# Kernel optimization log

Hardware: AMD Instinct MI355X
Metric: run time of the kernel (lower is better)

## Reference

```python
import jax, jax.numpy as jnp
import numpy as np

N = 50000       # nodes
E = 800000      # edges (before self-loops)
IN_DIM = 256
HIDDEN = 256
HEADS = 4
C1 = HIDDEN // HEADS  # 64 per-head channels in layer 1
OUT_DIM = 128
NEG_SLOPE = 0.2  # PyG GATConv default negative_slope


def setup_inputs() -> dict:
    key = jax.random.key(0)
    ks = jax.random.split(key, 10)
    x = jax.random.normal(ks[0], (N, IN_DIM), dtype=jnp.float32) * 0.1
    edge_index = jax.random.randint(ks[1], (2, E), 0, N, dtype=jnp.int64)
    # layer 1 params (GATConv: lin weight, att_src, att_dst, bias)
    W1 = jax.random.normal(ks[2], (IN_DIM, HEADS * C1), dtype=jnp.float32) * 0.05
    att_src1 = jax.random.normal(ks[3], (HEADS, C1), dtype=jnp.float32) * 0.05
    att_dst1 = jax.random.normal(ks[4], (HEADS, C1), dtype=jnp.float32) * 0.05
    bias1 = jnp.zeros((HEADS * C1,), dtype=jnp.float32)
    # layer 2 params (heads=1, concat=False)
    W2 = jax.random.normal(ks[5], (HIDDEN, OUT_DIM), dtype=jnp.float32) * 0.05
    att_src2 = jax.random.normal(ks[6], (1, OUT_DIM), dtype=jnp.float32) * 0.05
    att_dst2 = jax.random.normal(ks[7], (1, OUT_DIM), dtype=jnp.float32) * 0.05
    bias2 = jnp.zeros((OUT_DIM,), dtype=jnp.float32)
    return {"x": x, "edge_index": edge_index, "W1": W1, "att_src1": att_src1,
            "att_dst1": att_dst1, "bias1": bias1, "W2": W2, "att_src2": att_src2,
            "att_dst2": att_dst2, "bias2": bias2}


def gat_conv(x, src, dst, W, a_src, a_dst, bias, concat):
    # x: [N, F_in]; src/dst: [E'] (self-loops included); W: [F_in, H*C]
    H, C = a_src.shape
    h = (x @ W).reshape(-1, H, C)                      # [N, H, C]
    alpha_s = (h * a_src[None]).sum(-1)                # [N, H]
    alpha_d = (h * a_dst[None]).sum(-1)                # [N, H]
    e = jax.nn.leaky_relu(alpha_s[src] + alpha_d[dst], NEG_SLOPE)  # [E', H]
    # segment softmax over incoming edges of each destination node
    emax = jax.ops.segment_max(e, dst, num_segments=N)             # [N, H]
    ex = jnp.exp(e - emax[dst])
    denom = jax.ops.segment_sum(ex, dst, num_segments=N)           # [N, H]
    alpha = ex / (denom[dst] + 1e-16)                              # [E', H]
    msg = h[src] * alpha[:, :, None]                               # [E', H, C]
    out = jax.ops.segment_sum(msg, dst, num_segments=N)            # [N, H, C]
    if concat:
        out = out.reshape(N, H * C)
    else:
        out = out.mean(axis=1)
    return out + bias


def reference(x, edge_index, W1, att_src1, att_dst1, bias1, W2, att_src2, att_dst2, bias2):
    # PyG GATConv add_self_loops=True
    loops = jnp.arange(N, dtype=edge_index.dtype)
    src = jnp.concatenate([edge_index[0], loops])
    dst = jnp.concatenate([edge_index[1], loops])
    h = gat_conv(x, src, dst, W1, att_src1, att_dst1, bias1, concat=True)   # [N, 256]
    h = jax.nn.gelu(h, approximate=False)  # torch F.gelu default = exact erf
    # dropout inactive in eval mode
    out = gat_conv(h, src, dst, W2, att_src2, att_dst2, bias2, concat=False)  # [N, 128]
    return out
```

## Files before the change

### kernel.cpp

```cpp
#include <hip/hip_runtime.h>
#include <hip/hip_bf16.h>


#define IN_DIM   256
#define HID      256
#define HEADS    4
#define C1       64
#define OUT_DIM  128
#define NEG_SLOPE 0.2f

using short8 = __attribute__((ext_vector_type(8))) short;
using f32x4  = __attribute__((ext_vector_type(4))) float;
using uint2n = __attribute__((ext_vector_type(2))) unsigned int;

__device__ __forceinline__ float loadf(const void* p, size_t i, int isbf16) {
    return isbf16 ? __bfloat162float(((const __hip_bfloat16*)p)[i])
                  : ((const float*)p)[i];
}

__device__ __forceinline__ float leaky(float a) {
    return a > 0.f ? a : NEG_SLOPE * a;
}

__device__ __forceinline__ unsigned short f2bs(float f) {
    __hip_bfloat16 b = __float2bfloat16(f);
    return *reinterpret_cast<unsigned short*>(&b);
}

__device__ __forceinline__ float blo(unsigned u) {
    return __uint_as_float(u << 16);
}
__device__ __forceinline__ float bhi(unsigned u) {
    return __uint_as_float(u & 0xffff0000u);
}

__device__ __forceinline__ float gelu(float c) {
    return 0.5f * c * (1.0f + erff(c * 0.70710678f));
}


__global__ void prep_kernel(const void* x, int nx,
                            const void* W1, const void* as1w, const void* ad1w,
                            const void* b1, const void* W2, const void* as2w,
                            const void* ad2w, const void* b2,
                            float* as1wf, float* ad1wf, float* b1f,
                            float* as2wf, float* ad2wf, float* b2f,
                            int* flags) {
    const void* srcs[9] = {x, W1, as1w, ad1w, b1, W2, as2w, ad2w, b2};
    int ns[9] = {nx, IN_DIM * HID, HEADS * C1, HEADS * C1, HID,
                 HID * OUT_DIM, OUT_DIM, OUT_DIM, OUT_DIM};
    float* dsts[9] = {nullptr, nullptr, as1wf, ad1wf, b1f, nullptr, as2wf, ad2wf, b2f};

    int b = blockIdx.x;
    const unsigned short* u = (const unsigned short*)srcs[b];
    int n = ns[b];
    int nslots = n < 4096 ? n : 4096;
    int cnt = 0;
    for (int i = threadIdx.x; i < nslots; i += 256) {
        unsigned short a = u[i] & 0x7FFF;
        int e = a >> 7;
        if (a == 0 || (e >= 90 && e <= 140)) cnt++;
    }
    __shared__ int red[4];
    __shared__ int flagS;
    for (int o = 32; o > 0; o >>= 1) cnt += __shfl_down(cnt, o);
    if ((threadIdx.x & 63) == 0) red[threadIdx.x >> 6] = cnt;
    __syncthreads();
    if (threadIdx.x == 0) {
        int tot = red[0] + red[1] + red[2] + red[3];
        int f = (tot * 10 >= nslots * 8) ? 1 : 0;
        flags[b] = f;
        flagS = f;
    }
    __syncthreads();
    int f = flagS;
    float* d = dsts[b];
    if (d) {
        for (int i = threadIdx.x; i < n; i += 256) d[i] = loadf(srcs[b], i, f);
    }
}

__global__ void tpose_kernel(const void* W1, const void* W2,
                             const int* flags,
                             __hip_bfloat16* __restrict__ W1T,
                             __hip_bfloat16* __restrict__ W2T,
                             int* __restrict__ deg, int n) {
    int b = blockIdx.x;
    int t = threadIdx.x;
    int gi = b * 256 + t;
    if (gi < n) deg[gi] = 0;
    if (b < 256) {
        int i = b * 256 + t;
        int k = i >> 8, nn = i & 255;
        W1T[nn * 256 + k] = __float2bfloat16(loadf(W1, i, flags[1]));
    } else {
        int i = (b - 256) * 256 + t;
        int k = i >> 7, nn = i & 127;
        W2T[nn * 256 + k] = __float2bfloat16(loadf(W2, i, flags[5]));
    }
}


__global__ void count_kernel(const int* __restrict__ ei, int E, int EP,
                             int* __restrict__ deg) {
    int idx = blockIdx.x * blockDim.x + threadIdx.x;
    if (idx >= EP) return;
    int d = (idx < E) ? ei[E + idx] : (idx - E);
    atomicAdd(&deg[d], 1);
}

__global__ __launch_bounds__(256) void psum_kernel(const int* __restrict__ deg,
                                                   int* __restrict__ bsum, int n) {
    int i = blockIdx.x * 256 + threadIdx.x;
    int v = (i < n) ? deg[i] : 0;
#pragma unroll
    for (int o = 32; o > 0; o >>= 1) v += __shfl_down(v, o);
    __shared__ int red[4];
    if ((threadIdx.x & 63) == 0) red[threadIdx.x >> 6] = v;
    __syncthreads();
    if (threadIdx.x == 0) bsum[blockIdx.x] = red[0] + red[1] + red[2] + red[3];
}

__global__ __launch_bounds__(256) void wscan_kernel(int* __restrict__ deg,
                                                    const int* __restrict__ bsum,
                                                    int* __restrict__ offs,
                                                    float* __restrict__ z0,
                                                    float* __restrict__ z1,
                                                    int n) {
    __shared__ int sh[256];
    __shared__ int red[4];
    int b = blockIdx.x;
    int t = threadIdx.x;

    int pref = 0;
    for (int i = t; i < b; i += 256) pref += bsum[i];
#pragma unroll
    for (int o = 32; o > 0; o >>= 1) pref += __shfl_down(pref, o);
    if ((t & 63) == 0) red[t >> 6] = pref;
    __syncthreads();
    int bpref = red[0] + red[1] + red[2] + red[3];

    int i = b * 256 + t;
    int v = (i < n) ? deg[i] : 0;
    sh[t] = v;
    __syncthreads();
    for (int d = 1; d < 256; d <<= 1) {
        int u = (t >= d) ? sh[t - d] : 0;
        __syncthreads();
        sh[t] += u;
        __syncthreads();
    }
    int excl = sh[t] - v + bpref;
    if (i < n) {
        offs[i] = excl;
        deg[i]  = excl;
        z0[i] = 0.f;
        z1[i] = 0.f;
        if (i == n - 1) offs[n] = excl + v;
    }
}

__global__ void fill_kernel(const int* __restrict__ ei, int E, int EP,
                            int* __restrict__ cursor, int* __restrict__ ssrc,
                            int* __restrict__ sdst) {
    int idx = blockIdx.x * blockDim.x + threadIdx.x;
    if (idx >= EP) return;
    int src = (idx < E) ? ei[idx]     : (idx - E);
    int dst = (idx < E) ? ei[E + idx] : (idx - E);
    int pos = atomicAdd(&cursor[dst], 1);
    ssrc[pos] = src;
    sdst[pos] = dst;
}


__device__ __forceinline__ void store_out(float* C, size_t i, float v) { C[i] = v; }
__device__ __forceinline__ void store_out(__hip_bfloat16* C, size_t i, float v) {
    C[i] = __float2bfloat16(v);
}

template <typename OutT>
__global__ __launch_bounds__(256) void gemm_mfma(
    const void* __restrict__ A0, const int* aflagp,
    const __hip_bfloat16* __restrict__ BT,
    OutT* __restrict__ C, int M, int Nn, int K,
    const float* __restrict__ aswp, const float* __restrict__ adwp,
    float* __restrict__ asO, float* __restrict__ adO, int hstride) {
    constexpr int BM = 128, BN = 128, BK = 32;
    constexpr int LDK = BK + 8;
    __shared__ __hip_bfloat16 As[BM * LDK];
    __shared__ __hip_bfloat16 Bs[BN * LDK];

    const int Mb = (M + BM - 1) / BM;
    const int Nb = Nn / BN;
    int bmi, bni;
    if (Nb == 2) {
        int L = blockIdx.x;
        bmi = (L >> 4) * 8 + (L & 7);
        bni = (L >> 3) & 1;
        if (bmi >= Mb) return;
    } else {
        bmi = blockIdx.x;
        bni = 0;
        if (bmi >= Mb) return;
    }

    const int aflag = aflagp ? *aflagp : 1;
    const int tid  = threadIdx.x;
    const int lane = tid & 63;
    const int wv   = tid >> 6;
    const int wm   = (wv >> 1) * 64;
    const int wn   = (wv & 1) * 64;
    const int l15  = lane & 15;
    const int quad = lane >> 4;

    const int bm = bmi * BM;
    const int bn = bni * BN;

    f32x4 acc[4][4] = {};

    for (int k0 = 0; k0 < K; k0 += BK) {
#pragma unroll
        for (int i = 0; i < 2; ++i) {
            int c    = tid + i * 256;
            int row  = c >> 2;
            int koff = (c & 3) * 8;
            int grow = bm + row;
            short8 av = {};
            if (grow < M) {
                if (aflag) {
                    av = *(const short8*)((const __hip_bfloat16*)A0 +
                                          (size_t)grow * K + k0 + koff);
                } else {
                    const float* ap = (const float*)A0 + (size_t)grow * K + k0 + koff;
                    float4 f0 = *(const float4*)ap;
                    float4 f1 = *(const float4*)(ap + 4);
                    av[0] = (short)f2bs(f0.x); av[1] = (short)f2bs(f0.y);
                    av[2] = (short)f2bs(f0.z); av[3] = (short)f2bs(f0.w);
                    av[4] = (short)f2bs(f1.x); av[5] = (short)f2bs(f1.y);
                    av[6] = (short)f2bs(f1.z); av[7] = (short)f2bs(f1.w);
                }
            }
            *(short8*)&As[row * LDK + koff] = av;
            short8 bv = *(const short8*)(BT + (size_t)(bn + row) * K + k0 + koff);
            *(short8*)&Bs[row * LDK + koff] = bv;
        }
        __syncthreads();

        short8 af[4], bf[4];
#pragma unroll
        for (int f = 0; f < 4; ++f) {
            af[f] = *(const short8*)&As[(wm + f * 16 + l15) * LDK + quad * 8];
            bf[f] = *(const short8*)&Bs[(wn + f * 16 + l15) * LDK + quad * 8];
        }
#pragma unroll
        for (int fm = 0; fm < 4; ++fm)
#pragma unroll
            for (int fn = 0; fn < 4; ++fn)
                acc[fm][fn] = __builtin_amdgcn_mfma_f32_16x16x32_bf16(
                    af[fm], bf[fn], acc[fm][fn], 0, 0, 0);
        __syncthreads();
    }

#pragma unroll
    for (int fm = 0; fm < 4; ++fm) {
#pragma unroll
        for (int r = 0; r < 4; ++r) {
            int grow = bm + wm + fm * 16 + quad * 4 + r;
            if (grow >= M) continue;
#pragma unroll
            for (int fn = 0; fn < 4; ++fn) {
                int gcol = bn + wn + fn * 16 + l15;
                store_out(C, (size_t)grow * Nn + gcol, acc[fm][fn][r]);
            }
        }
    }

    if (aswp) {
        float aw[4], dw[4];
#pragma unroll
        for (int fn = 0; fn < 4; ++fn) {
            int gcol = bn + wn + fn * 16 + l15;
            aw[fn] = aswp[gcol];
            dw[fn] = adwp[gcol];
        }
        int head = (bn + wn) >> 6;
#pragma unroll
        for (int fm = 0; fm < 4; ++fm) {
#pragma unroll
            for (int r = 0; r < 4; ++r) {
                int grow = bm + wm + fm * 16 + quad * 4 + r;
                float sa = acc[fm][0][r] * aw[0] + acc[fm][1][r] * aw[1]
                         + acc[fm][2][r] * aw[2] + acc[fm][3][r] * aw[3];
                float sd = acc[fm][0][r] * dw[0] + acc[fm][1][r] * dw[1]
                         + acc[fm][2][r] * dw[2] + acc[fm][3][r] * dw[3];
#pragma unroll
                for (int o = 8; o > 0; o >>= 1) {
                    sa += __shfl_xor(sa, o);
                    sd += __shfl_xor(sd, o);
                }
                if (l15 == 0 && grow < M) {
                    if (hstride == 4) {
                        asO[grow * 4 + head] = sa;
                        adO[grow * 4 + head] = sd;
                    } else {
                        atomicAdd(&asO[grow], sa);
                        atomicAdd(&adO[grow], sd);
                    }
                }
            }
        }
    }
}


__global__ void wcalc2_kernel(const int* __restrict__ ssrc,
                              const int* __restrict__ sdst,
                              const float* __restrict__ as2,
                              const float* __restrict__ ad2,
                              float* __restrict__ w2, int EP) {
    int i = blockIdx.x * blockDim.x + threadIdx.x;
    if (i >= EP) return;
    w2[i] = __expf(leaky(as2[ssrc[i]] + ad2[sdst[i]]));
}


__global__ __launch_bounds__(256) void agg1g_kernel(
    const uint4* __restrict__ h1, const float* __restrict__ as1,
    const float* __restrict__ ad1, const int* __restrict__ offs,
    const int* __restrict__ ssrc, const float* __restrict__ bias1,
    uint4* __restrict__ g, int n) {
    int lane = threadIdx.x & 63;
    int wv   = threadIdx.x >> 6;
    int half = lane >> 5;
    int l32  = lane & 31;
    int v = blockIdx.x * 8 + wv * 2 + half;
    if (v >= n) return;
    int head = l32 >> 3;
    int start = offs[v], end = offs[v + 1];
    float adv = ad1[v * 4 + head];

    float aL0=0,aH0=0,aL1=0,aH1=0,aL2=0,aH2=0,aL3=0,aH3=0,den=0;
    int i = start;
    for (; i + 8 <= end; i += 8) {
        int s[8];
#pragma unroll
        for (int j = 0; j < 8; ++j) s[j] = ssrc[i + j];
        float e[8]; uint4 p[8];
#pragma unroll
        for (int j = 0; j < 8; ++j) {
            e[j] = as1[s[j] * 4 + head];
            p[j] = h1[(size_t)s[j] * 32 + l32];
        }
        float w[8];
#pragma unroll
        for (int j = 0; j < 8; ++j) {
            w[j] = __expf(leaky(e[j] + adv));
            den += w[j];
        }
#pragma unroll
        for (int j = 0; j < 8; ++j) {
            aL0 = fmaf(w[j], blo(p[j].x), aL0); aH0 = fmaf(w[j], bhi(p[j].x), aH0);
            aL1 = fmaf(w[j], blo(p[j].y), aL1); aH1 = fmaf(w[j], bhi(p[j].y), aH1);
            aL2 = fmaf(w[j], blo(p[j].z), aL2); aH2 = fmaf(w[j], bhi(p[j].z), aH2);
            aL3 = fmaf(w[j], blo(p[j].w), aL3); aH3 = fmaf(w[j], bhi(p[j].w), aH3);
        }
    }
    for (; i + 4 <= end; i += 4) {
        int s0 = ssrc[i], s1 = ssrc[i+1], s2 = ssrc[i+2], s3 = ssrc[i+3];
        float e0 = as1[s0*4+head], e1 = as1[s1*4+head];
        float e2 = as1[s2*4+head], e3 = as1[s3*4+head];
        uint4 p0 = h1[(size_t)s0*32 + l32];
        uint4 p1 = h1[(size_t)s1*32 + l32];
        uint4 p2 = h1[(size_t)s2*32 + l32];
        uint4 p3 = h1[(size_t)s3*32 + l32];
        float w0 = __expf(leaky(e0+adv));
        float w1 = __expf(leaky(e1+adv));
        float w2 = __expf(leaky(e2+adv));
        float w3 = __expf(leaky(e3+adv));
        den += (w0+w1)+(w2+w3);
        aL0 = fmaf(w0, blo(p0.x), fmaf(w1, blo(p1.x), fmaf(w2, blo(p2.x), fmaf(w3, blo(p3.x), aL0))));
        aH0 = fmaf(w0, bhi(p0.x), fmaf(w1, bhi(p1.x), fmaf(w2, bhi(p2.x), fmaf(w3, bhi(p3.x), aH0))));
        aL1 = fmaf(w0, blo(p0.y), fmaf(w1, blo(p1.y), fmaf(w2, blo(p2.y), fmaf(w3, blo(p3.y), aL1))));
        aH1 = fmaf(w0, bhi(p0.y), fmaf(w1, bhi(p1.y), fmaf(w2, bhi(p2.y), fmaf(w3, bhi(p3.y), aH1))));
        aL2 = fmaf(w0, blo(p0.z), fmaf(w1, blo(p1.z), fmaf(w2, blo(p2.z), fmaf(w3, blo(p3.z), aL2))));
        aH2 = fmaf(w0, bhi(p0.z), fmaf(w1, bhi(p1.z), fmaf(w2, bhi(p2.z), fmaf(w3, bhi(p3.z), aH2))));
        aL3 = fmaf(w0, blo(p0.w), fmaf(w1, blo(p1.w), fmaf(w2, blo(p2.w), fmaf(w3, blo(p3.w), aL3))));
        aH3 = fmaf(w0, bhi(p0.w), fmaf(w1, bhi(p1.w), fmaf(w2, bhi(p2.w), fmaf(w3, bhi(p3.w), aH3))));
    }
    for (; i < end; ++i) {
        int s = ssrc[i];
        float w = __expf(leaky(as1[s*4+head] + adv));
        uint4 p = h1[(size_t)s*32 + l32];
        den += w;
        aL0 = fmaf(w, blo(p.x), aL0); aH0 = fmaf(w, bhi(p.x), aH0);
        aL1 = fmaf(w, blo(p.y), aL1); aH1 = fmaf(w, bhi(p.y), aH1);
        aL2 = fmaf(w, blo(p.z), aL2); aH2 = fmaf(w, bhi(p.z), aH2);
        aL3 = fmaf(w, blo(p.w), aL3); aH3 = fmaf(w, bhi(p.w), aH3);
    }
    float inv = 1.f / (den + 1e-16f);
    float4 bq0 = *(const float4*)&bias1[8 * l32];
    float4 bq1 = *(const float4*)&bias1[8 * l32 + 4];
    float c0 = gelu(aL0*inv + bq0.x), c1 = gelu(aH0*inv + bq0.y);
    float c2 = gelu(aL1*inv + bq0.z), c3 = gelu(aH1*inv + bq0.w);
    float c4 = gelu(aL2*inv + bq1.x), c5 = gelu(aH2*inv + bq1.y);
    float c6 = gelu(aL3*inv + bq1.z), c7 = gelu(aH3*inv + bq1.w);
    uint4 r;
    r.x = (unsigned)f2bs(c0) | ((unsigned)f2bs(c1) << 16);
    r.y = (unsigned)f2bs(c2) | ((unsigned)f2bs(c3) << 16);
    r.z = (unsigned)f2bs(c4) | ((unsigned)f2bs(c5) << 16);
    r.w = (unsigned)f2bs(c6) | ((unsigned)f2bs(c7) << 16);
    g[(size_t)v * 32 + l32] = r;
}

__global__ __launch_bounds__(256) void agg2s_kernel(
    const uint4* __restrict__ h2, const float* __restrict__ w2,
    const int* __restrict__ offs, const int* __restrict__ ssrc,
    const float* __restrict__ bias2,
    void* __restrict__ out, const int* outflagp, int n) {
    int lane = threadIdx.x & 63;
    int wv   = threadIdx.x >> 6;
    int sub  = lane >> 4;
    int l16  = lane & 15;
    int v = blockIdx.x * 16 + wv * 4 + sub;
    if (v >= n) return;
    int start = offs[v], end = offs[v + 1];

    float a0=0,a1=0,a2=0,a3=0,a4=0,a5=0,a6=0,a7=0,den=0;
    int i = start;
    for (; i + 8 <= end; i += 8) {
        int s[8];
#pragma unroll
        for (int j = 0; j < 8; ++j) s[j] = ssrc[i + j];
        float w[8]; uint4 p[8];
#pragma unroll
        for (int j = 0; j < 8; ++j) {
            w[j] = w2[i + j];
            p[j] = h2[(size_t)s[j] * 16 + l16];
        }
#pragma unroll
        for (int j = 0; j < 8; ++j) {
            den += w[j];
            a0 = fmaf(w[j], blo(p[j].x), a0); a1 = fmaf(w[j], bhi(p[j].x), a1);
            a2 = fmaf(w[j], blo(p[j].y), a2); a3 = fmaf(w[j], bhi(p[j].y), a3);
            a4 = fmaf(w[j], blo(p[j].z), a4); a5 = fmaf(w[j], bhi(p[j].z), a5);
            a6 = fmaf(w[j], blo(p[j].w), a6); a7 = fmaf(w[j], bhi(p[j].w), a7);
        }
    }
    for (; i < end; ++i) {
        float w = w2[i];
        uint4 p = h2[(size_t)ssrc[i] * 16 + l16];
        den += w;
        a0 = fmaf(w, blo(p.x), a0); a1 = fmaf(w, bhi(p.x), a1);
        a2 = fmaf(w, blo(p.y), a2); a3 = fmaf(w, bhi(p.y), a3);
        a4 = fmaf(w, blo(p.z), a4); a5 = fmaf(w, bhi(p.z), a5);
        a6 = fmaf(w, blo(p.w), a6); a7 = fmaf(w, bhi(p.w), a7);
    }
    float inv = 1.f / (den + 1e-16f);
    int cb = 8 * l16;
    float4 bq0 = *(const float4*)&bias2[cb];
    float4 bq1 = *(const float4*)&bias2[cb + 4];
    float o0 = a0*inv + bq0.x, o1 = a1*inv + bq0.y;
    float o2 = a2*inv + bq0.z, o3 = a3*inv + bq0.w;
    float o4 = a4*inv + bq1.x, o5 = a5*inv + bq1.y;
    float o6 = a6*inv + bq1.z, o7 = a7*inv + bq1.w;
    if (*outflagp) {
        uint4 rv;
        rv.x = (unsigned)f2bs(o0) | ((unsigned)f2bs(o1) << 16);
        rv.y = (unsigned)f2bs(o2) | ((unsigned)f2bs(o3) << 16);
        rv.z = (unsigned)f2bs(o4) | ((unsigned)f2bs(o5) << 16);
        rv.w = (unsigned)f2bs(o6) | ((unsigned)f2bs(o7) << 16);
        *(uint4*)((unsigned short*)out + (size_t)v * 128 + cb) = rv;
    } else {
        float* op = (float*)out + (size_t)v * 128 + cb;
        *(float4*)op       = make_float4(o0, o1, o2, o3);
        *(float4*)(op + 4) = make_float4(o4, o5, o6, o7);
    }
}


static inline char* alignp(char* p, size_t a) {
    return (char*)(((uintptr_t)p + a - 1) & ~(uintptr_t)(a - 1));
}

extern "C" void kernel_launch(void* const* d_in, const int* in_sizes, int n_in,
                              void* d_out, int out_size, void* d_ws, size_t ws_size,
                              hipStream_t stream) {
    const void* x    = d_in[0];
    const int*  ei   = (const int*)d_in[1];
    const void* W1   = d_in[2];
    const void* as1w = d_in[3];
    const void* ad1w = d_in[4];
    const void* b1   = d_in[5];
    const void* W2   = d_in[6];
    const void* as2w = d_in[7];
    const void* ad2w = d_in[8];
    const void* b2   = d_in[9];

    const int N  = out_size / OUT_DIM;
    const int E  = in_sizes[1] / 2;
    const int EP = E + N;
    const int NB = (N + 255) / 256;
    const int Mb = (N + 127) / 128;

    char* p = (char*)d_ws;
    __hip_bfloat16* h1  = (__hip_bfloat16*)p;
    __hip_bfloat16* h2b = (__hip_bfloat16*)p;  p += (size_t)N * HID * 2;
    __hip_bfloat16* g   = (__hip_bfloat16*)p;  p += (size_t)N * HID * 2;
    float* as1wf = (float*)p;                 p += 256 * 4;
    float* ad1wf = (float*)p;                 p += 256 * 4;
    float* b1f   = (float*)p;                 p += 256 * 4;
    float* as2wf = (float*)p;                 p += 128 * 4;
    float* ad2wf = (float*)p;                 p += 128 * 4;
    float* b2f   = (float*)p;                 p += 128 * 4;
    float* as1   = (float*)p;                 p += (size_t)N * HEADS * 4;
    float* ad1   = (float*)p;                 p += (size_t)N * HEADS * 4;
    float* as2   = (float*)p;                 p += (size_t)N * 4;
    float* ad2   = (float*)p;                 p += (size_t)N * 4;
    int*   flags = (int*)p;                   p += 16 * 4;
    int*   deg   = (int*)p;                   p += (size_t)N * 4;
    int*   offs  = (int*)p;                   p += (size_t)(N + 1) * 4;
    int*   bsum  = (int*)p;                   p += (size_t)1024 * 4;
    int*   ssrc  = (int*)p;                   p += (size_t)EP * 4;
    int*   sdst  = (int*)p;                   p += (size_t)EP * 4;
    float* w2e   = (float*)p;                 p += (size_t)EP * 4;
    p = alignp(p, 64);
    __hip_bfloat16* W1T = (__hip_bfloat16*)p; p += (size_t)HID * IN_DIM * 2;
    __hip_bfloat16* W2T = (__hip_bfloat16*)p; p += (size_t)OUT_DIM * HID * 2;

    prep_kernel<<<9, 256, 0, stream>>>(x, in_sizes[0], W1, as1w, ad1w, b1,
                                       W2, as2w, ad2w, b2,
                                       as1wf, ad1wf, b1f, as2wf, ad2wf, b2f,
                                       flags);
    tpose_kernel<<<384, 256, 0, stream>>>(W1, W2, flags, W1T, W2T, deg, N);

    {
        int blk = 256, grd = (EP + blk - 1) / blk;
        count_kernel<<<grd, blk, 0, stream>>>(ei, E, EP, deg);
        psum_kernel<<<NB, 256, 0, stream>>>(deg, bsum, N);
        wscan_kernel<<<NB, 256, 0, stream>>>(deg, bsum, offs, as2, ad2, N);
        fill_kernel<<<grd, blk, 0, stream>>>(ei, E, EP, deg, ssrc, sdst);
    }

    int g1blocks = ((Mb + 7) / 8) * 16;
    gemm_mfma<__hip_bfloat16><<<g1blocks, 256, 0, stream>>>(
        x, flags + 0, W1T, h1, N, HID, IN_DIM,
        as1wf, ad1wf, as1, ad1, 4);
    agg1g_kernel<<<(N + 7) / 8, 256, 0, stream>>>((const uint4*)h1, as1, ad1, offs, ssrc,
                                                  b1f, (uint4*)g, N);

    gemm_mfma<__hip_bfloat16><<<Mb, 256, 0, stream>>>(
        g, nullptr, W2T, h2b, N, OUT_DIM, HID,
        as2wf, ad2wf, as2, ad2, 1);
    wcalc2_kernel<<<(EP + 255) / 256, 256, 0, stream>>>(ssrc, sdst, as2, ad2, w2e, EP);
    agg2s_kernel<<<(N + 15) / 16, 256, 0, stream>>>((const uint4*)h2b, w2e, offs, ssrc,
                                                    b2f, d_out, flags + 0, N);
}
```

Baseline: 359.3 us.

## Fuse preprocessing kernels, merge CSR fill into GEMM1, inline layer-2 edge weights

Merges prep and transpose into one launch, with each transpose block recomputing the dtype flag locally. The psum pass is dropped by having each scan block re-reduce all preceding degrees directly. The CSR fill is co-scheduled with GEMM1 blocks in a single grid, and the sdst array is removed. The wcalc2 pass and its per-edge weight buffer are removed by computing exp(leaky(as2[s]+ad2[v])) inside agg2s. This cuts launch count and global traffic, at the cost of redundant prefix reads in the scan (quadratic across blocks) and extra exp work during aggregation.

```diff
diff --git a/kernel.cpp b/kernel.cpp
--- a/kernel.cpp
+++ b/kernel.cpp
@@ -39,64 +39,81 @@
 }
 
 
-__global__ void prep_kernel(const void* x, int nx,
-                            const void* W1, const void* as1w, const void* ad1w,
-                            const void* b1, const void* W2, const void* as2w,
-                            const void* ad2w, const void* b2,
-                            float* as1wf, float* ad1wf, float* b1f,
-                            float* as2wf, float* ad2wf, float* b2f,
-                            int* flags) {
-    const void* srcs[9] = {x, W1, as1w, ad1w, b1, W2, as2w, ad2w, b2};
-    int ns[9] = {nx, IN_DIM * HID, HEADS * C1, HEADS * C1, HID,
-                 HID * OUT_DIM, OUT_DIM, OUT_DIM, OUT_DIM};
-    float* dsts[9] = {nullptr, nullptr, as1wf, ad1wf, b1f, nullptr, as2wf, ad2wf, b2f};
-
+__global__ void prep_tpose_kernel(const void* x, int nx,
+                                  const void* W1, const void* as1w, const void* ad1w,
+                                  const void* b1, const void* W2, const void* as2w,
+                                  const void* ad2w, const void* b2,
+                                  float* as1wf, float* ad1wf, float* b1f,
+                                  float* as2wf, float* ad2wf, float* b2f,
+                                  int* flags,
+                                  __hip_bfloat16* __restrict__ W1T,
+                                  __hip_bfloat16* __restrict__ W2T,
+                                  int* __restrict__ deg, int n) {
+    __shared__ int red[4];
+    __shared__ int flagS;
     int b = blockIdx.x;
-    const unsigned short* u = (const unsigned short*)srcs[b];
-    int n = ns[b];
-    int nslots = n < 4096 ? n : 4096;
+    int t = threadIdx.x;
+
+    if (b < 9) {
+        const void* srcs[9] = {x, W1, as1w, ad1w, b1, W2, as2w, ad2w, b2};
+        int ns[9] = {nx, IN_DIM * HID, HEADS * C1, HEADS * C1, HID,
+                     HID * OUT_DIM, OUT_DIM, OUT_DIM, OUT_DIM};
+        float* dsts[9] = {nullptr, nullptr, as1wf, ad1wf, b1f, nullptr, as2wf, ad2wf, b2f};
+
+        const unsigned short* u = (const unsigned short*)srcs[b];
+        int nn = ns[b];
+        int nslots = nn < 4096 ? nn : 4096;
+        int cnt = 0;
+        for (int i = t; i < nslots; i += 256) {
+            unsigned short a = u[i] & 0x7FFF;
+            int e = a >> 7;
+            if (a == 0 || (e >= 90 && e <= 140)) cnt++;
+        }
+        for (int o = 32; o > 0; o >>= 1) cnt += __shfl_down(cnt, o);
+        if ((t & 63) == 0) red[t >> 6] = cnt;
+        __syncthreads();
+        if (t == 0) {
+            int tot = red[0] + red[1] + red[2] + red[3];
+            int f = (tot * 10 >= nslots * 8) ? 1 : 0;
+            flags[b] = f;
+            flagS = f;
+        }
+        __syncthreads();
+        int f = flagS;
+        float* d = dsts[b];
+        if (d) {
+            for (int i = t; i < nn; i += 256) d[i] = loadf(srcs[b], i, f);
+        }
+        return;
+    }
+
+    int bb = b - 9;
+    int gi = bb * 256 + t;
+    if (gi < n) deg[gi] = 0;
+
+    const void* src = (bb < 256) ? W1 : W2;
+    const unsigned short* u = (const unsigned short*)src;
     int cnt = 0;
-    for (int i = threadIdx.x; i < nslots; i += 256) {
+    for (int i = t; i < 4096; i += 256) {
         unsigned short a = u[i] & 0x7FFF;
         int e = a >> 7;
         if (a == 0 || (e >= 90 && e <= 140)) cnt++;
     }
-    __shared__ int red[4];
-    __shared__ int flagS;
     for (int o = 32; o > 0; o >>= 1) cnt += __shfl_down(cnt, o);
-    if ((threadIdx.x & 63) == 0) red[threadIdx.x >> 6] = cnt;
+    if ((t & 63) == 0) red[t >> 6] = cnt;
     __syncthreads();
-    if (threadIdx.x == 0) {
-        int tot = red[0] + red[1] + red[2] + red[3];
-        int f = (tot * 10 >= nslots * 8) ? 1 : 0;
-        flags[b] = f;
-        flagS = f;
-    }
+    if (t == 0) flagS = ((red[0] + red[1] + red[2] + red[3]) * 10 >= 4096 * 8) ? 1 : 0;
     __syncthreads();
     int f = flagS;
-    float* d = dsts[b];
-    if (d) {
-        for (int i = threadIdx.x; i < n; i += 256) d[i] = loadf(srcs[b], i, f);
-    }
-}
-
-__global__ void tpose_kernel(const void* W1, const void* W2,
-                             const int* flags,
-                             __hip_bfloat16* __restrict__ W1T,
-                             __hip_bfloat16* __restrict__ W2T,
-                             int* __restrict__ deg, int n) {
-    int b = blockIdx.x;
-    int t = threadIdx.x;
-    int gi = b * 256 + t;
-    if (gi < n) deg[gi] = 0;
-    if (b < 256) {
-        int i = b * 256 + t;
+
+    if (bb < 256) {
+        int i = bb * 256 + t;
         int k = i >> 8, nn = i & 255;
-        W1T[nn * 256 + k] = __float2bfloat16(loadf(W1, i, flags[1]));
+        W1T[nn * 256 + k] = __float2bfloat16(loadf(W1, i, f));
     } else {
-        int i = (b - 256) * 256 + t;
+        int i = (bb - 256) * 256 + t;
         int k = i >> 7, nn = i & 127;
-        W2T[nn * 256 + k] = __float2bfloat16(loadf(W2, i, flags[5]));
+        W2T[nn * 256 + k] = __float2bfloat16(loadf(W2, i, f));
     }
 }
 
@@ -109,21 +126,9 @@
     atomicAdd(&deg[d], 1);
 }
 
-__global__ __launch_bounds__(256) void psum_kernel(const int* __restrict__ deg,
-                                                   int* __restrict__ bsum, int n) {
-    int i = blockIdx.x * 256 + threadIdx.x;
-    int v = (i < n) ? deg[i] : 0;
-#pragma unroll
-    for (int o = 32; o > 0; o >>= 1) v += __shfl_down(v, o);
-    __shared__ int red[4];
-    if ((threadIdx.x & 63) == 0) red[threadIdx.x >> 6] = v;
-    __syncthreads();
-    if (threadIdx.x == 0) bsum[blockIdx.x] = red[0] + red[1] + red[2] + red[3];
-}
-
-__global__ __launch_bounds__(256) void wscan_kernel(int* __restrict__ deg,
-                                                    const int* __restrict__ bsum,
+__global__ __launch_bounds__(256) void wscan_kernel(const int* __restrict__ deg,
                                                     int* __restrict__ offs,
+                                                    int* __restrict__ cur,
                                                     float* __restrict__ z0,
                                                     float* __restrict__ z1,
                                                     int n) {
@@ -131,16 +136,17 @@
     __shared__ int red[4];
     int b = blockIdx.x;
     int t = threadIdx.x;
+    int base = b * 256;
 
     int pref = 0;
-    for (int i = t; i < b; i += 256) pref += bsum[i];
+    for (int i = t; i < base; i += 256) pref += deg[i];
 #pragma unroll
     for (int o = 32; o > 0; o >>= 1) pref += __shfl_down(pref, o);
     if ((t & 63) == 0) red[t >> 6] = pref;
     __syncthreads();
     int bpref = red[0] + red[1] + red[2] + red[3];
 
-    int i = b * 256 + t;
+    int i = base + t;
     int v = (i < n) ? deg[i] : 0;
     sh[t] = v;
     __syncthreads();
@@ -153,25 +159,13 @@
     int excl = sh[t] - v + bpref;
     if (i < n) {
         offs[i] = excl;
-        deg[i]  = excl;
+        cur[i]  = excl;
         z0[i] = 0.f;
         z1[i] = 0.f;
         if (i == n - 1) offs[n] = excl + v;
     }
 }
 
-__global__ void fill_kernel(const int* __restrict__ ei, int E, int EP,
-                            int* __restrict__ cursor, int* __restrict__ ssrc,
-                            int* __restrict__ sdst) {
-    int idx = blockIdx.x * blockDim.x + threadIdx.x;
-    if (idx >= EP) return;
-    int src = (idx < E) ? ei[idx]     : (idx - E);
-    int dst = (idx < E) ? ei[E + idx] : (idx - E);
-    int pos = atomicAdd(&cursor[dst], 1);
-    ssrc[pos] = src;
-    sdst[pos] = dst;
-}
-
 
 __device__ __forceinline__ void store_out(float* C, size_t i, float v) { C[i] = v; }
 __device__ __forceinline__ void store_out(__hip_bfloat16* C, size_t i, float v) {
@@ -179,32 +173,19 @@
 }
 
 template <typename OutT>
-__global__ __launch_bounds__(256) void gemm_mfma(
-    const void* __restrict__ A0, const int* aflagp,
-    const __hip_bfloat16* __restrict__ BT,
-    OutT* __restrict__ C, int M, int Nn, int K,
-    const float* __restrict__ aswp, const float* __restrict__ adwp,
-    float* __restrict__ asO, float* __restrict__ adO, int hstride) {
+__device__ void gemm_body(const void* __restrict__ A0, int aflag,
+                          const __hip_bfloat16* __restrict__ BT,
+                          OutT* __restrict__ C, int M, int Nn, int K,
+                          int bmi, int bni,
+                          const float* __restrict__ aswp,
+                          const float* __restrict__ adwp,
+                          float* __restrict__ asO, float* __restrict__ adO,
+                          int hstride) {
     constexpr int BM = 128, BN = 128, BK = 32;
     constexpr int LDK = BK + 8;
     __shared__ __hip_bfloat16 As[BM * LDK];
     __shared__ __hip_bfloat16 Bs[BN * LDK];
 
-    const int Mb = (M + BM - 1) / BM;
-    const int Nb = Nn / BN;
-    int bmi, bni;
-    if (Nb == 2) {
-        int L = blockIdx.x;
-        bmi = (L >> 4) * 8 + (L & 7);
-        bni = (L >> 3) & 1;
-        if (bmi >= Mb) return;
-    } else {
-        bmi = blockIdx.x;
-        bni = 0;
-        if (bmi >= Mb) return;
-    }
-
-    const int aflag = aflagp ? *aflagp : 1;
     const int tid  = threadIdx.x;
     const int lane = tid & 63;
     const int wv   = tid >> 6;
@@ -312,15 +293,40 @@
     }
 }
 
-
-__global__ void wcalc2_kernel(const int* __restrict__ ssrc,
-                              const int* __restrict__ sdst,
-                              const float* __restrict__ as2,
-                              const float* __restrict__ ad2,
-                              float* __restrict__ w2, int EP) {
-    int i = blockIdx.x * blockDim.x + threadIdx.x;
-    if (i >= EP) return;
-    w2[i] = __expf(leaky(as2[ssrc[i]] + ad2[sdst[i]]));
+__global__ __launch_bounds__(256) void gemm1_fill_kernel(
+    const void* __restrict__ x, const int* __restrict__ flags,
+    const __hip_bfloat16* __restrict__ W1T, __hip_bfloat16* __restrict__ h1,
+    int M, const float* __restrict__ as1wf, const float* __restrict__ ad1wf,
+    float* __restrict__ as1, float* __restrict__ ad1,
+    int g1blocks, int Mb,
+    const int* __restrict__ ei, int E, int EP,
+    int* __restrict__ cursor, int* __restrict__ ssrc) {
+    int bid = blockIdx.x;
+    if (bid < g1blocks) {
+        int bmi = (bid >> 4) * 8 + (bid & 7);
+        int bni = (bid >> 3) & 1;
+        if (bmi >= Mb) return;
+        gemm_body<__hip_bfloat16>(x, flags[0], W1T, h1, M, HID, IN_DIM,
+                                  bmi, bni, as1wf, ad1wf, as1, ad1, 4);
+    } else {
+        int idx = (bid - g1blocks) * 256 + threadIdx.x;
+        if (idx >= EP) return;
+        int src = (idx < E) ? ei[idx]     : (idx - E);
+        int dst = (idx < E) ? ei[E + idx] : (idx - E);
+        int pos = atomicAdd(&cursor[dst], 1);
+        ssrc[pos] = src;
+    }
+}
+
+__global__ __launch_bounds__(256) void gemm2_kernel(
+    const __hip_bfloat16* __restrict__ g, const __hip_bfloat16* __restrict__ W2T,
+    __hip_bfloat16* __restrict__ h2, int M,
+    const float* __restrict__ as2wf, const float* __restrict__ ad2wf,
+    float* __restrict__ as2, float* __restrict__ ad2, int Mb) {
+    int bmi = blockIdx.x;
+    if (bmi >= Mb) return;
+    gemm_body<__hip_bfloat16>(g, 1, W2T, h2, M, OUT_DIM, HID,
+                              bmi, 0, as2wf, ad2wf, as2, ad2, 1);
 }
 
 
@@ -413,9 +419,9 @@
 }
 
 __global__ __launch_bounds__(256) void agg2s_kernel(
-    const uint4* __restrict__ h2, const float* __restrict__ w2,
-    const int* __restrict__ offs, const int* __restrict__ ssrc,
-    const float* __restrict__ bias2,
+    const uint4* __restrict__ h2, const float* __restrict__ as2,
+    const float* __restrict__ ad2, const int* __restrict__ offs,
+    const int* __restrict__ ssrc, const float* __restrict__ bias2,
     void* __restrict__ out, const int* outflagp, int n) {
     int lane = threadIdx.x & 63;
     int wv   = threadIdx.x >> 6;
@@ -424,6 +430,7 @@
     int v = blockIdx.x * 16 + wv * 4 + sub;
     if (v >= n) return;
     int start = offs[v], end = offs[v + 1];
+    float adv = ad2[v];
 
     float a0=0,a1=0,a2=0,a3=0,a4=0,a5=0,a6=0,a7=0,den=0;
     int i = start;
@@ -431,15 +438,20 @@
         int s[8];
 #pragma unroll
         for (int j = 0; j < 8; ++j) s[j] = ssrc[i + j];
-        float w[8]; uint4 p[8];
+        float e[8]; uint4 p[8];
 #pragma unroll
         for (int j = 0; j < 8; ++j) {
-            w[j] = w2[i + j];
+            e[j] = as2[s[j]];
             p[j] = h2[(size_t)s[j] * 16 + l16];
         }
+        float w[8];
 #pragma unroll
         for (int j = 0; j < 8; ++j) {
+            w[j] = __expf(leaky(e[j] + adv));
             den += w[j];
+        }
+#pragma unroll
+        for (int j = 0; j < 8; ++j) {
             a0 = fmaf(w[j], blo(p[j].x), a0); a1 = fmaf(w[j], bhi(p[j].x), a1);
             a2 = fmaf(w[j], blo(p[j].y), a2); a3 = fmaf(w[j], bhi(p[j].y), a3);
             a4 = fmaf(w[j], blo(p[j].z), a4); a5 = fmaf(w[j], bhi(p[j].z), a5);
@@ -447,8 +459,9 @@
         }
     }
     for (; i < end; ++i) {
-        float w = w2[i];
-        uint4 p = h2[(size_t)ssrc[i] * 16 + l16];
+        int s = ssrc[i];
+        float w = __expf(leaky(as2[s] + adv));
+        uint4 p = h2[(size_t)s * 16 + l16];
         den += w;
         a0 = fmaf(w, blo(p.x), a0); a1 = fmaf(w, bhi(p.x), a1);
         a2 = fmaf(w, blo(p.y), a2); a3 = fmaf(w, bhi(p.y), a3);
@@ -518,40 +531,28 @@
     float* ad2   = (float*)p;                 p += (size_t)N * 4;
     int*   flags = (int*)p;                   p += 16 * 4;
     int*   deg   = (int*)p;                   p += (size_t)N * 4;
+    int*   cur   = (int*)p;                   p += (size_t)N * 4;
     int*   offs  = (int*)p;                   p += (size_t)(N + 1) * 4;
-    int*   bsum  = (int*)p;                   p += (size_t)1024 * 4;
     int*   ssrc  = (int*)p;                   p += (size_t)EP * 4;
-    int*   sdst  = (int*)p;                   p += (size_t)EP * 4;
-    float* w2e   = (float*)p;                 p += (size_t)EP * 4;
     p = alignp(p, 64);
     __hip_bfloat16* W1T = (__hip_bfloat16*)p; p += (size_t)HID * IN_DIM * 2;
     __hip_bfloat16* W2T = (__hip_bfloat16*)p; p += (size_t)OUT_DIM * HID * 2;
 
-    prep_kernel<<<9, 256, 0, stream>>>(x, in_sizes[0], W1, as1w, ad1w, b1,
-                                       W2, as2w, ad2w, b2,
-                                       as1wf, ad1wf, b1f, as2wf, ad2wf, b2f,
-                                       flags);
-    tpose_kernel<<<384, 256, 0, stream>>>(W1, W2, flags, W1T, W2T, deg, N);
-
-    {
-        int blk = 256, grd = (EP + blk - 1) / blk;
-        count_kernel<<<grd, blk, 0, stream>>>(ei, E, EP, deg);
-        psum_kernel<<<NB, 256, 0, stream>>>(deg, bsum, N);
-        wscan_kernel<<<NB, 256, 0, stream>>>(deg, bsum, offs, as2, ad2, N);
-        fill_kernel<<<grd, blk, 0, stream>>>(ei, E, EP, deg, ssrc, sdst);
-    }
-
-    int g1blocks = ((Mb + 7) / 8) * 16;
-    gemm_mfma<__hip_bfloat16><<<g1blocks, 256, 0, stream>>>(
-        x, flags + 0, W1T, h1, N, HID, IN_DIM,
-        as1wf, ad1wf, as1, ad1, 4);
+    const int grd = (EP + 255) / 256;
+    const int g1blocks = ((Mb + 7) / 8) * 16;
+
+    prep_tpose_kernel<<<393, 256, 0, stream>>>(x, in_sizes[0], W1, as1w, ad1w, b1,
+                                               W2, as2w, ad2w, b2,
+                                               as1wf, ad1wf, b1f, as2wf, ad2wf, b2f,
+                                               flags, W1T, W2T, deg, N);
+    count_kernel<<<grd, 256, 0, stream>>>(ei, E, EP, deg);
+    wscan_kernel<<<NB, 256, 0, stream>>>(deg, offs, cur, as2, ad2, N);
+    gemm1_fill_kernel<<<g1blocks + grd, 256, 0, stream>>>(
+        x, flags, W1T, h1, N, as1wf, ad1wf, as1, ad1, g1blocks, Mb,
+        ei, E, EP, cur, ssrc);
     agg1g_kernel<<<(N + 7) / 8, 256, 0, stream>>>((const uint4*)h1, as1, ad1, offs, ssrc,
                                                   b1f, (uint4*)g, N);
-
-    gemm_mfma<__hip_bfloat16><<<Mb, 256, 0, stream>>>(
-        g, nullptr, W2T, h2b, N, OUT_DIM, HID,
-        as2wf, ad2wf, as2, ad2, 1);
-    wcalc2_kernel<<<(EP + 255) / 256, 256, 0, stream>>>(ssrc, sdst, as2, ad2, w2e, EP);
-    agg2s_kernel<<<(N + 15) / 16, 256, 0, stream>>>((const uint4*)h2b, w2e, offs, ssrc,
+    gemm2_kernel<<<Mb, 256, 0, stream>>>(g, W2T, h2b, N, as2wf, ad2wf, as2, ad2, Mb);
+    agg2s_kernel<<<(N + 15) / 16, 256, 0, stream>>>((const uint4*)h2b, as2, ad2, offs, ssrc,
                                                     b2f, d_out, flags + 0, N);
 }
```

After: 399.1 us. +11.1%, slower.
